# Optimization experiments

Hardware: AMD Instinct MI355X
Metric: run time of the kernel (lower is better)

## Reference

```python
import math
import jax, jax.numpy as jnp
import numpy as np

SCALE = 64.0
MARGIN = 0.5
COS_M = math.cos(MARGIN)
SIN_M = math.sin(MARGIN)
TH = math.cos(math.pi - MARGIN)
MM = math.sin(math.pi - MARGIN) * MARGIN
EPS = 1e-12  # F.normalize default eps

B, D, C = 2048, 512, 100000


def setup_inputs() -> dict:
    key = jax.random.key(0)
    k1, k2, k3 = jax.random.split(key, 3)
    embeddings = jax.random.normal(k1, (B, D), dtype=jnp.float32)
    labels = jax.random.randint(k2, (B,), 0, C, dtype=jnp.int64)
    # xavier-uniform-like init for weight [C, D]
    limit = math.sqrt(6.0 / (C + D))
    weight = jax.random.uniform(k3, (C, D), dtype=jnp.float32, minval=-limit, maxval=limit)
    return {"embeddings": embeddings, "labels": labels, "weight": weight}


def _l2norm(x):
    n = jnp.linalg.norm(x, axis=-1, keepdims=True)
    return x / jnp.maximum(n, EPS)


def reference(embeddings, labels, weight):
    cosine = _l2norm(embeddings) @ _l2norm(weight).T  # [B, C]
    sine = jnp.sqrt(jnp.clip(1.0 - cosine * cosine, 0.0, None))
    phi = cosine * COS_M - sine * SIN_M
    phi = jnp.where(cosine > TH, phi, cosine - MM)
    # one-hot blend without materializing a separate one-hot tensor
    col = jnp.arange(cosine.shape[1])[None, :]
    is_target = col == labels[:, None]  # [B, C] bool
    logits = jnp.where(is_target, phi, cosine)
    return logits * SCALE
```

## Files before the change

kernel.cpp:

```cpp
#include <hip/hip_runtime.h>
#include <hip/hip_bf16.h>
#include <math.h>

constexpr int Bq = 2048;
constexpr int Dq = 512;
constexpr int Cq = 100000;
constexpr int NPAD = 100096;

constexpr float SCALE = 64.0f;
constexpr float COS_M = 0.8775825618903728f;
constexpr float SIN_M = 0.479425538604203f;
constexpr float THR   = -0.8775825618903728f;
constexpr float MM    = 0.2397127693021015f;

typedef __attribute__((ext_vector_type(8))) __bf16 bf16x8;
typedef __attribute__((ext_vector_type(4))) float f32x4;

typedef const __attribute__((address_space(1))) unsigned int guint;
typedef __attribute__((address_space(3))) unsigned int suint;

__device__ __forceinline__ void gload_lds16(const unsigned short* g, unsigned short* lds)
{
    __builtin_amdgcn_global_load_lds((guint*)g, (suint*)lds, 16, 0, 0);
}

__device__ __forceinline__ unsigned int pack_bf16x2(float lo, float hi)
{
    __hip_bfloat16 h0 = __float2bfloat16(lo);
    __hip_bfloat16 h1 = __float2bfloat16(hi);
    return ((unsigned int)(*(unsigned short*)&h1) << 16) |
           (unsigned int)(*(unsigned short*)&h0);
}

__global__ __launch_bounds__(256) void normalize_rows_kernel(
    const float* __restrict__ in, unsigned short* __restrict__ out, int nrows)
{
    const int w = threadIdx.x >> 6, lane = threadIdx.x & 63;
    const int row = blockIdx.x * 4 + w;
    float4 a = {0.f, 0.f, 0.f, 0.f}, b = a;
    if (row < nrows) {
        const float4* src = reinterpret_cast<const float4*>(in + (size_t)row * Dq);
        a = src[lane];
        b = src[lane + 64];
    }
    float ss = a.x * a.x + a.y * a.y + a.z * a.z + a.w * a.w
             + b.x * b.x + b.y * b.y + b.z * b.z + b.w * b.w;
    #pragma unroll
    for (int off = 32; off > 0; off >>= 1) ss += __shfl_down(ss, off);
    ss = __shfl(ss, 0);
    const float invn = 1.0f / fmaxf(sqrtf(ss), 1e-12f);

    uint2* out64 = reinterpret_cast<uint2*>(out + (size_t)row * Dq);
    uint2 pa, pb;
    pa.x = pack_bf16x2(a.x * invn, a.y * invn);
    pa.y = pack_bf16x2(a.z * invn, a.w * invn);
    pb.x = pack_bf16x2(b.x * invn, b.y * invn);
    pb.y = pack_bf16x2(b.z * invn, b.w * invn);
    out64[lane] = pa;
    out64[lane + 64] = pb;
}

__global__ __launch_bounds__(256, 2) void arc_gemm_kernel(
    const unsigned short* __restrict__ A,
    const unsigned short* __restrict__ Bn,
    const int* __restrict__ labels,
    float* __restrict__ out)
{
    extern __shared__ unsigned short lds[];

    const int cpx = (int)gridDim.x >> 3;
    const int bid = ((int)blockIdx.x & 7) * cpx + ((int)blockIdx.x >> 3);
    const int tm = bid & 15;
    const int tn = bid >> 4;
    const int m0 = tm * 128, n0 = tn * 128;

    const int t = threadIdx.x;
    const int w = t >> 6, lane = t & 63;
    const int wr = (w >> 1) * 64;
    const int wc = (w & 1) * 64;
    const int fr = lane & 15, kg = lane >> 4;
    const int s7 = fr & 7;
    const int c0 = (kg ^ s7) * 8;
    const int c1 = ((4 + kg) ^ s7) * 8;

    const int trow = t >> 3;
    const int tch = ((t & 7) ^ (trow & 7)) * 8;
    const unsigned short* gA = A  + (size_t)(m0 + trow) * Dq + tch;
    const unsigned short* gB = Bn + (size_t)(n0 + trow) * Dq + tch;
    const int dstA = trow * 64 + (t & 7) * 8;

#define STAGE_A(buf, s, kts) gload_lds16(gA + (size_t)(s) * 32 * Dq + (size_t)(kts) * 64, \
                                         &lds[(buf) * 16384 + (s) * 2048 + dstA])
#define STAGE_B(buf, s, kts) gload_lds16(gB + (size_t)(s) * 32 * Dq + (size_t)(kts) * 64, \
                                         &lds[(buf) * 16384 + 8192 + (s) * 2048 + dstA])
#define BARRIER() do { __builtin_amdgcn_sched_barrier(0); __builtin_amdgcn_s_barrier(); } while (0)

    f32x4 acc[4][4];
    #pragma unroll
    for (int i = 0; i < 4; ++i)
        #pragma unroll
        for (int j = 0; j < 4; ++j) acc[i][j] = {0.f, 0.f, 0.f, 0.f};

    STAGE_A(0, 0, 0); STAGE_A(0, 1, 0); STAGE_A(0, 2, 0); STAGE_A(0, 3, 0);
    STAGE_B(0, 0, 0); STAGE_B(0, 1, 0); STAGE_B(0, 2, 0); STAGE_B(0, 3, 0);
    STAGE_B(1, 0, 1); STAGE_B(1, 1, 1); STAGE_B(1, 2, 1); STAGE_B(1, 3, 1);
    STAGE_A(1, 0, 1); STAGE_A(1, 2, 1);
    asm volatile("s_waitcnt vmcnt(6)" ::: "memory");
    __builtin_amdgcn_s_barrier();

    const int arow = (wr + fr) * 64;
    const int brow = 8192 + (wc + fr) * 64;

#define LDAQ(dst, q) do { \
    dst[0] = *reinterpret_cast<const bf16x8*>(&lds[cbo + arow + (q) * 1024 + c0]); \
    dst[1] = *reinterpret_cast<const bf16x8*>(&lds[cbo + arow + (q) * 1024 + c1]); \
} while (0)
#define LDB() do { \
    _Pragma("unroll") for (int ni = 0; ni < 4; ++ni) { \
        bfr[ni][0] = *reinterpret_cast<const bf16x8*>(&lds[cbo + brow + ni * 1024 + c0]); \
        bfr[ni][1] = *reinterpret_cast<const bf16x8*>(&lds[cbo + brow + ni * 1024 + c1]); } \
} while (0)
#define MFMA_PAIR(q0, a0, q1, a1) do { \
    __builtin_amdgcn_s_setprio(1); \
    _Pragma("unroll") for (int ks = 0; ks < 2; ++ks) \
    _Pragma("unroll") for (int ni = 0; ni < 4; ++ni) { \
        acc[(q0)][ni] = __builtin_amdgcn_mfma_f32_16x16x32_bf16( \
            bfr[ni][ks], a0[ks], acc[(q0)][ni], 0, 0, 0); \
        acc[(q1)][ni] = __builtin_amdgcn_mfma_f32_16x16x32_bf16( \
            bfr[ni][ks], a1[ks], acc[(q1)][ni], 0, 0, 0); } \
    __builtin_amdgcn_s_setprio(0); \
} while (0)

    #pragma unroll
    for (int kt = 0; kt < 8; ++kt) {
        const int cb = kt & 1, nb = cb ^ 1;
        const int cbo = cb * 16384;
        bf16x8 bfr[4][2];
        bf16x8 af0[2], af1[2], af2[2], af3[2];
        LDB(); LDAQ(af0, 0); LDAQ(af1, 1);
        if (kt < 7) { STAGE_A(nb, 1, kt + 1); STAGE_A(nb, 3, kt + 1); }
        BARRIER();
        MFMA_PAIR(0, af0, 1, af1);
        BARRIER();
        LDAQ(af2, 2); LDAQ(af3, 3);
        if (kt < 6) {
            STAGE_B(cb, 0, kt + 2); STAGE_B(cb, 1, kt + 2);
            STAGE_B(cb, 2, kt + 2); STAGE_B(cb, 3, kt + 2);
            STAGE_A(cb, 0, kt + 2); STAGE_A(cb, 2, kt + 2);
        }
        BARRIER();
        MFMA_PAIR(2, af2, 3, af3);
        if (kt < 6) asm volatile("s_waitcnt vmcnt(6)" ::: "memory");
        else        asm volatile("s_waitcnt vmcnt(0)" ::: "memory");
        BARRIER();
    }

    float* lf = reinterpret_cast<float*>(lds);
    #pragma unroll
    for (int mi = 0; mi < 4; ++mi) {
        const int lrow = wr + mi * 16 + fr;
        const int lab = labels[m0 + lrow];
        #pragma unroll
        for (int ni = 0; ni < 4; ++ni) {
            const int col0 = wc + ni * 16 + kg * 4;
            const int gcol0 = n0 + col0;
            f32x4 v = acc[mi][ni];
            #pragma unroll
            for (int r = 0; r < 4; ++r) {
                if (gcol0 + r == lab) {
                    float c = v[r];
                    float sine = sqrtf(fmaxf(1.0f - c * c, 0.0f));
                    float phi = c * COS_M - sine * SIN_M;
                    v[r] = (c > THR) ? phi : (c - MM);
                }
            }
            v *= SCALE;
            *reinterpret_cast<f32x4*>(&lf[lrow * 132 + col0]) = v;
        }
    }
    __syncthreads();
    const int cc = lane & 31, rh = lane >> 5;
    #pragma unroll
    for (int s = 0; s < 16; ++s) {
        const int lrow = (w * 16 + s) * 2 + rh;
        f32x4 v = *reinterpret_cast<const f32x4*>(&lf[lrow * 132 + cc * 4]);
        const int gcol0 = n0 + cc * 4;
        if (gcol0 < Cq)
            __builtin_nontemporal_store(
                v, reinterpret_cast<f32x4*>(out + (size_t)(m0 + lrow) * Cq + gcol0));
    }
#undef STAGE_A
#undef STAGE_B
#undef BARRIER
#undef LDAQ
#undef LDB
#undef MFMA_PAIR
}

extern "C" void kernel_launch(void* const* d_in, const int* in_sizes, int n_in,
                              void* d_out, int out_size, void* d_ws, size_t ws_size,
                              hipStream_t stream)
{
    const float* emb    = (const float*)d_in[0];
    const int*   labels = (const int*)d_in[1];
    const float* weight = (const float*)d_in[2];
    float* out = (float*)d_out;

    unsigned short* Abf = (unsigned short*)d_ws;
    unsigned short* Bbf = Abf + (size_t)Bq * Dq;

    normalize_rows_kernel<<<Bq / 4, 256, 0, stream>>>(emb, Abf, Bq);
    normalize_rows_kernel<<<NPAD / 4, 256, 0, stream>>>(weight, Bbf, Cq);
    arc_gemm_kernel<<<16 * (NPAD / 128), 256, 67584, stream>>>(Abf, Bbf, labels, out);
}
```

Baseline: 325.2 us.

## Process two N tiles per block, storing first tile's results during second GEMM

Each workgroup now computes two adjacent 128-column output tiles, which halves the grid. The first tile's epilogue results are held in registers and written to global memory with nontemporal stores spread through the second tile's K loop. The aim is to overlap the large output write traffic with MFMA work and to amortize per-block launch and prologue cost. The trade-offs are 64 extra VGPRs for the held results and first-tile stores that go straight from registers in the MFMA fragment layout instead of through coalesced LDS rows. Only the second tile keeps the column bounds check.

After: 328.0 us. About the same (+0.9%).

```diff
diff --git a/kernel.cpp b/kernel.cpp
--- a/kernel.cpp
+++ b/kernel.cpp
@@ -71,8 +71,8 @@
     const int cpx = (int)gridDim.x >> 3;
     const int bid = ((int)blockIdx.x & 7) * cpx + ((int)blockIdx.x >> 3);
     const int tm = bid & 15;
-    const int tn = bid >> 4;
-    const int m0 = tm * 128, n0 = tn * 128;
+    const int pn = bid >> 4;
+    const int m0 = tm * 128, n0 = pn * 256;
 
     const int t = threadIdx.x;
     const int w = t >> 6, lane = t & 63;
@@ -85,28 +85,21 @@
 
     const int trow = t >> 3;
     const int tch = ((t & 7) ^ (trow & 7)) * 8;
-    const unsigned short* gA = A  + (size_t)(m0 + trow) * Dq + tch;
-    const unsigned short* gB = Bn + (size_t)(n0 + trow) * Dq + tch;
+    const unsigned short* gA = A + (size_t)(m0 + trow) * Dq + tch;
+    const unsigned short* gBt = Bn + (size_t)(n0 + trow) * Dq + tch;
     const int dstA = trow * 64 + (t & 7) * 8;
 
 #define STAGE_A(buf, s, kts) gload_lds16(gA + (size_t)(s) * 32 * Dq + (size_t)(kts) * 64, \
                                          &lds[(buf) * 16384 + (s) * 2048 + dstA])
-#define STAGE_B(buf, s, kts) gload_lds16(gB + (size_t)(s) * 32 * Dq + (size_t)(kts) * 64, \
+#define STAGE_B(buf, s, kts) gload_lds16(gBt + (size_t)(s) * 32 * Dq + (size_t)(kts) * 64, \
                                          &lds[(buf) * 16384 + 8192 + (s) * 2048 + dstA])
 #define BARRIER() do { __builtin_amdgcn_sched_barrier(0); __builtin_amdgcn_s_barrier(); } while (0)
-
-    f32x4 acc[4][4];
-    #pragma unroll
-    for (int i = 0; i < 4; ++i)
-        #pragma unroll
-        for (int j = 0; j < 4; ++j) acc[i][j] = {0.f, 0.f, 0.f, 0.f};
-
-    STAGE_A(0, 0, 0); STAGE_A(0, 1, 0); STAGE_A(0, 2, 0); STAGE_A(0, 3, 0);
-    STAGE_B(0, 0, 0); STAGE_B(0, 1, 0); STAGE_B(0, 2, 0); STAGE_B(0, 3, 0);
-    STAGE_B(1, 0, 1); STAGE_B(1, 1, 1); STAGE_B(1, 2, 1); STAGE_B(1, 3, 1);
-    STAGE_A(1, 0, 1); STAGE_A(1, 2, 1);
-    asm volatile("s_waitcnt vmcnt(6)" ::: "memory");
-    __builtin_amdgcn_s_barrier();
+#define PROLOGUE() do { \
+    STAGE_A(0, 0, 0); STAGE_A(0, 1, 0); STAGE_A(0, 2, 0); STAGE_A(0, 3, 0); \
+    STAGE_B(0, 0, 0); STAGE_B(0, 1, 0); STAGE_B(0, 2, 0); STAGE_B(0, 3, 0); \
+    STAGE_B(1, 0, 1); STAGE_B(1, 1, 1); STAGE_B(1, 2, 1); STAGE_B(1, 3, 1); \
+    STAGE_A(1, 0, 1); STAGE_A(1, 2, 1); \
+} while (0)
 
     const int arow = (wr + fr) * 64;
     const int brow = 8192 + (wc + fr) * 64;
@@ -131,30 +124,79 @@
     __builtin_amdgcn_s_setprio(0); \
 } while (0)
 
-    #pragma unroll
-    for (int kt = 0; kt < 8; ++kt) {
-        const int cb = kt & 1, nb = cb ^ 1;
-        const int cbo = cb * 16384;
-        bf16x8 bfr[4][2];
-        bf16x8 af0[2], af1[2], af2[2], af3[2];
-        LDB(); LDAQ(af0, 0); LDAQ(af1, 1);
-        if (kt < 7) { STAGE_A(nb, 1, kt + 1); STAGE_A(nb, 3, kt + 1); }
-        BARRIER();
-        MFMA_PAIR(0, af0, 1, af1);
-        BARRIER();
-        LDAQ(af2, 2); LDAQ(af3, 3);
-        if (kt < 6) {
-            STAGE_B(cb, 0, kt + 2); STAGE_B(cb, 1, kt + 2);
-            STAGE_B(cb, 2, kt + 2); STAGE_B(cb, 3, kt + 2);
-            STAGE_A(cb, 0, kt + 2); STAGE_A(cb, 2, kt + 2);
+#define KT_STEP(kt, DO_ST) { \
+        const int cb = (kt) & 1, nb = cb ^ 1; \
+        const int cbo = cb * 16384; \
+        bf16x8 bfr[4][2]; \
+        bf16x8 af0[2], af1[2], af2[2], af3[2]; \
+        if (DO_ST) { \
+            __builtin_nontemporal_store(sv[(kt) >> 1][((kt) & 1) * 2], \
+                reinterpret_cast<f32x4*>(obase + (size_t)((kt) >> 1) * 16 * Cq + (((kt) & 1) * 2) * 16)); \
+            __builtin_nontemporal_store(sv[(kt) >> 1][((kt) & 1) * 2 + 1], \
+                reinterpret_cast<f32x4*>(obase + (size_t)((kt) >> 1) * 16 * Cq + (((kt) & 1) * 2 + 1) * 16)); \
+        } \
+        LDB(); LDAQ(af0, 0); LDAQ(af1, 1); \
+        if ((kt) < 7) { STAGE_A(nb, 1, (kt) + 1); STAGE_A(nb, 3, (kt) + 1); } \
+        BARRIER(); \
+        MFMA_PAIR(0, af0, 1, af1); \
+        BARRIER(); \
+        LDAQ(af2, 2); LDAQ(af3, 3); \
+        if ((kt) < 6) { \
+            STAGE_B(cb, 0, (kt) + 2); STAGE_B(cb, 1, (kt) + 2); \
+            STAGE_B(cb, 2, (kt) + 2); STAGE_B(cb, 3, (kt) + 2); \
+            STAGE_A(cb, 0, (kt) + 2); STAGE_A(cb, 2, (kt) + 2); \
+        } \
+        BARRIER(); \
+        MFMA_PAIR(2, af2, 3, af3); \
+        if ((kt) < 6) asm volatile("s_waitcnt vmcnt(6)" ::: "memory"); \
+        else          asm volatile("s_waitcnt vmcnt(0)" ::: "memory"); \
+        BARRIER(); \
+    }
+
+    f32x4 acc[4][4];
+    #pragma unroll
+    for (int i = 0; i < 4; ++i)
+        #pragma unroll
+        for (int j = 0; j < 4; ++j) acc[i][j] = {0.f, 0.f, 0.f, 0.f};
+
+    f32x4 sv[4][4];
+    float* obase = out + (size_t)(m0 + wr + fr) * Cq + n0 + wc + kg * 4;
+
+    PROLOGUE();
+    asm volatile("s_waitcnt vmcnt(6)" ::: "memory");
+    __builtin_amdgcn_s_barrier();
+    KT_STEP(0, 0) KT_STEP(1, 0) KT_STEP(2, 0) KT_STEP(3, 0)
+    KT_STEP(4, 0) KT_STEP(5, 0) KT_STEP(6, 0) KT_STEP(7, 0)
+
+    gBt += (size_t)128 * Dq;
+    PROLOGUE();
+    #pragma unroll
+    for (int mi = 0; mi < 4; ++mi) {
+        const int lab = labels[m0 + wr + mi * 16 + fr];
+        #pragma unroll
+        for (int ni = 0; ni < 4; ++ni) {
+            const int gcol0 = n0 + wc + ni * 16 + kg * 4;
+            f32x4 v = acc[mi][ni];
+            #pragma unroll
+            for (int r = 0; r < 4; ++r) {
+                if (gcol0 + r == lab) {
+                    float c = v[r];
+                    float sine = sqrtf(fmaxf(1.0f - c * c, 0.0f));
+                    float phi = c * COS_M - sine * SIN_M;
+                    v[r] = (c > THR) ? phi : (c - MM);
+                }
+            }
+            sv[mi][ni] = v * SCALE;
+            acc[mi][ni] = {0.f, 0.f, 0.f, 0.f};
         }
-        BARRIER();
-        MFMA_PAIR(2, af2, 3, af3);
-        if (kt < 6) asm volatile("s_waitcnt vmcnt(6)" ::: "memory");
-        else        asm volatile("s_waitcnt vmcnt(0)" ::: "memory");
-        BARRIER();
-    }
-
+    }
+    asm volatile("s_waitcnt vmcnt(6)" ::: "memory");
+    __builtin_amdgcn_s_barrier();
+
+    KT_STEP(0, 1) KT_STEP(1, 1) KT_STEP(2, 1) KT_STEP(3, 1)
+    KT_STEP(4, 1) KT_STEP(5, 1) KT_STEP(6, 1) KT_STEP(7, 1)
+
+    const int n0e = n0 + 128;
     float* lf = reinterpret_cast<float*>(lds);
     #pragma unroll
     for (int mi = 0; mi < 4; ++mi) {
@@ -163,7 +205,7 @@
         #pragma unroll
         for (int ni = 0; ni < 4; ++ni) {
             const int col0 = wc + ni * 16 + kg * 4;
-            const int gcol0 = n0 + col0;
+            const int gcol0 = n0e + col0;
             f32x4 v = acc[mi][ni];
             #pragma unroll
             for (int r = 0; r < 4; ++r) {
@@ -184,7 +226,7 @@
     for (int s = 0; s < 16; ++s) {
         const int lrow = (w * 16 + s) * 2 + rh;
         f32x4 v = *reinterpret_cast<const f32x4*>(&lf[lrow * 132 + cc * 4]);
-        const int gcol0 = n0 + cc * 4;
+        const int gcol0 = n0e + cc * 4;
         if (gcol0 < Cq)
             __builtin_nontemporal_store(
                 v, reinterpret_cast<f32x4*>(out + (size_t)(m0 + lrow) * Cq + gcol0));
@@ -192,9 +234,11 @@
 #undef STAGE_A
 #undef STAGE_B
 #undef BARRIER
+#undef PROLOGUE
 #undef LDAQ
 #undef LDB
 #undef MFMA_PAIR
+#undef KT_STEP
 }
 
 extern "C" void kernel_launch(void* const* d_in, const int* in_sizes, int n_in,
@@ -211,5 +255,5 @@
 
     normalize_rows_kernel<<<Bq / 4, 256, 0, stream>>>(emb, Abf, Bq);
     normalize_rows_kernel<<<NPAD / 4, 256, 0, stream>>>(weight, Bbf, Cq);
-    arc_gemm_kernel<<<16 * (NPAD / 128), 256, 67584, stream>>>(Abf, Bbf, labels, out);
-}
+    arc_gemm_kernel<<<16 * (NPAD / 256), 256, 67584, stream>>>(Abf, Bbf, labels, out);
+}
```
